# Performance work log

Measured on AMD Instinct MI355X. Metric: run time of the kernel, lower is better.

The kernel has to match this reference:

```python
import jax, jax.numpy as jnp
import numpy as np

B, S, L, D = 16, 1024, 512, 1024
H = 8
DH = D // H
WD = 256          # word/type embedding dim
VOCAB = 1000      # type vocab
NEG = -1e30


def setup_inputs() -> dict:
    key = jax.random.key(0)
    ks = jax.random.split(key, 16)
    inv = 1.0 / np.sqrt(D)
    return {
        "encoder_outs": jax.random.normal(ks[0], (B, S, D), dtype=jnp.float32),
        "to_sem": jax.random.randint(ks[1], (B, L), 0, S, dtype=jnp.int64),
        "to_sem_type": jax.random.randint(ks[2], (B, L), 0, VOCAB, dtype=jnp.int64),
        "sem_syn": jax.random.randint(ks[3], (B, S), 0, L + 1, dtype=jnp.int64),
        "wq": jax.random.normal(ks[4], (D, D), dtype=jnp.float32) * inv,
        "bq": jnp.zeros((D,), dtype=jnp.float32),
        "wk": jax.random.normal(ks[5], (D, D), dtype=jnp.float32) * inv,
        "bk": jnp.zeros((D,), dtype=jnp.float32),
        "wv": jax.random.normal(ks[6], (D, D), dtype=jnp.float32) * inv,
        "bv": jnp.zeros((D,), dtype=jnp.float32),
        "wo": jax.random.normal(ks[7], (D, D), dtype=jnp.float32) * inv,
        "bo": jnp.zeros((D,), dtype=jnp.float32),
        "type_emb": jax.random.normal(ks[8], (VOCAB, WD), dtype=jnp.float32),
        "w_proj": jax.random.normal(ks[9], (D, D + WD), dtype=jnp.float32) / np.sqrt(D + WD),
        "b_proj": jnp.zeros((D,), dtype=jnp.float32),
        "bias_root": jax.random.normal(ks[10], (1, 1, D), dtype=jnp.float32),
    }


def _forward(encoder_outs, to_sem, to_sem_type, sem_syn,
             wq, bq, wk, bk, wv, bv, wo, bo,
             type_emb, w_proj, b_proj, bias_root):
    bsz, len_sem = to_sem.shape
    src_len = encoder_outs.shape[1]

    # batch_index_select: gather the encoder states at semantic head positions
    sem_vec = jnp.take_along_axis(encoder_outs, to_sem[:, :, None], axis=1)  # [B,L,D]

    # Vectorized mask build (replaces the Python loop + scatter):
    # buf[b,i,j] = (sem_syn[b,j] == i+1) or (j == to_sem[b,i])
    ids = jnp.arange(1, len_sem + 1, dtype=sem_syn.dtype)
    aligned = sem_syn[:, None, :] == ids[None, :, None]                       # [B,L,S]
    self_pos = jnp.arange(src_len)[None, None, :] == to_sem[:, :, None]       # [B,L,S]
    allow = aligned | self_pos                                                # [B,L,S]

    # fairseq-style MHA: q scaled by head_dim**-0.5, in/out proj with bias
    q = (sem_vec @ wq.T + bq) * (DH ** -0.5)
    k = encoder_outs @ wk.T + bk
    v = encoder_outs @ wv.T + bv
    q = q.reshape(bsz, len_sem, H, DH)
    k = k.reshape(bsz, src_len, H, DH)
    v = v.reshape(bsz, src_len, H, DH)

    scores = jnp.einsum("blhd,bshd->bhls", q, k)                              # [B,H,L,S]
    scores = jnp.where(allow[:, None, :, :], scores, NEG)
    attn = jax.nn.softmax(scores, axis=-1)
    ctx = jnp.einsum("bhls,bshd->blhd", attn, v).reshape(bsz, len_sem, D)
    sem_vec = ctx @ wo.T + bo                                                 # [B,L,D]

    # arg/type embedding + concat + projection
    type_vec = type_emb[to_sem_type]                                          # [B,L,WD]
    embedding = jnp.concatenate([sem_vec, type_vec], axis=-1) @ w_proj.T + b_proj

    root = jnp.broadcast_to(bias_root, (bsz, 1, D))
    return embedding, jnp.concatenate([root, embedding], axis=1)


def reference(encoder_outs, to_sem, to_sem_type, sem_syn,
              wq, bq, wk, bk, wv, bv, wo, bo,
              type_emb, w_proj, b_proj, bias_root):
    return _forward(encoder_outs, to_sem, to_sem_type, sem_syn,
                    wq, bq, wk, bk, wv, bv, wo, bo,
                    type_emb, w_proj, b_proj, bias_root)
```

## Files before the change

kernel.cpp:

```cpp
#include <hip/hip_runtime.h>

typedef unsigned short u16;
typedef unsigned int   u32;
typedef unsigned long long u64;
typedef __bf16 bf16x8 __attribute__((ext_vector_type(8)));
typedef float  f32x4  __attribute__((ext_vector_type(4)));

#define B_  16
#define S_  1024
#define L_  512
#define D_  1024
#define H_  8
#define WD_ 256
#define KP_ (D_ + WD_)

__device__ __forceinline__ u16 f2bf(float f) {
    u32 u = __float_as_uint(f);
    return (u16)((u + 0x7FFFu + ((u >> 16) & 1u)) >> 16);
}
__device__ __forceinline__ float bf2f(u16 h) {
    return __uint_as_float(((u32)h) << 16);
}
__device__ __forceinline__ void gload16(const void* g, void* l) {
    __builtin_amdgcn_global_load_lds(
        (const __attribute__((address_space(1))) u32*)(unsigned long long)(g),
        (__attribute__((address_space(3))) u32*)(unsigned long long)(l),
        16, 0, 0);
}

__global__ __launch_bounds__(256) void conv_s(const float* __restrict__ x,
                                              u16* __restrict__ y, int n, float s) {
    const int i = (blockIdx.x * 256 + threadIdx.x) * 4;
    if (i < n) {
        const float4 v = *(const float4*)(x + i);
        ushort4 o;
        o.x = f2bf(v.x * s); o.y = f2bf(v.y * s); o.z = f2bf(v.z * s); o.w = f2bf(v.w * s);
        *(ushort4*)(y + i) = o;
    }
}

__global__ __launch_bounds__(256) void conv3_k(
    const float* __restrict__ wk, const float* __restrict__ wv,
    const float* __restrict__ wq, const float* __restrict__ te,
    const float* __restrict__ bk, const float* __restrict__ bv,
    const float* __restrict__ bq,
    u16* __restrict__ wkvq, u16* __restrict__ te_bf,
    float* __restrict__ bkvq, float qs)
{
    const int bid = blockIdx.x;
    if (bid < 3072) {
        const int plane = bid >> 10;
        const int i = ((bid & 1023) * 256 + threadIdx.x) * 4;
        const float* src = plane == 0 ? wk : (plane == 1 ? wv : wq);
        const float s = plane == 2 ? qs : 1.0f;
        const float4 v = *(const float4*)(src + i);
        ushort4 o;
        o.x = f2bf(v.x * s); o.y = f2bf(v.y * s); o.z = f2bf(v.z * s); o.w = f2bf(v.w * s);
        *(ushort4*)(wkvq + (size_t)plane * 1048576 + i) = o;
    } else if (bid < 3322) {
        const int i = ((bid - 3072) * 256 + threadIdx.x) * 4;
        if (i < 256000) {
            const float4 v = *(const float4*)(te + i);
            ushort4 o;
            o.x = f2bf(v.x); o.y = f2bf(v.y); o.z = f2bf(v.z); o.w = f2bf(v.w);
            *(ushort4*)(te_bf + i) = o;
        }
    } else {
        const int i = (bid - 3322) * 1024 + threadIdx.x * 4;
        #pragma unroll
        for (int j = 0; j < 4; ++j) {
            const int idx = i + j;
            bkvq[idx] = (idx < 1024) ? bk[idx]
                      : (idx < 2048 ? bv[idx - 1024] : bq[idx - 2048] * qs);
        }
    }
}

__global__ __launch_bounds__(256) void convT_k(const float* __restrict__ x, u16* __restrict__ y) {
    __shared__ float tile[64][65];
    const int t0 = (blockIdx.x & 15) * 64;
    const int k0 = (blockIdx.x >> 4) * 64;
    const int tr = threadIdx.x >> 4;
    const int tc = threadIdx.x & 15;
    #pragma unroll
    for (int i = 0; i < 4; ++i) {
        const int r = tr + i * 16;
        const float4 v = *(const float4*)(x + (size_t)(t0 + r) * 1024 + k0 + tc * 4);
        tile[r][tc * 4 + 0] = v.x; tile[r][tc * 4 + 1] = v.y;
        tile[r][tc * 4 + 2] = v.z; tile[r][tc * 4 + 3] = v.w;
    }
    __syncthreads();
    #pragma unroll
    for (int i = 0; i < 4; ++i) {
        const int r = tr + i * 16;
        ushort4 o;
        o.x = f2bf(tile[tc * 4 + 0][r]);
        o.y = f2bf(tile[tc * 4 + 1][r]);
        o.z = f2bf(tile[tc * 4 + 2][r]);
        o.w = f2bf(tile[tc * 4 + 3][r]);
        *(ushort4*)(y + (size_t)(k0 + r) * 1024 + t0 + tc * 4) = o;
    }
}

__global__ __launch_bounds__(256) void convP_k(const float* __restrict__ x,
                                               u16* __restrict__ wp1, u16* __restrict__ wfin) {
    const int i = (blockIdx.x * 256 + threadIdx.x) * 4;
    if (i >= 1024 * 1280) return;
    const int n = i / 1280, c = i % 1280;
    const float4 v = *(const float4*)(x + i);
    ushort4 o;
    o.x = f2bf(v.x); o.y = f2bf(v.y); o.z = f2bf(v.z); o.w = f2bf(v.w);
    if (c < 1024) *(ushort4*)(wp1 + (size_t)n * 1024 + c) = o;
    else          *(ushort4*)(wfin + (size_t)n * 1280 + c) = o;
}

__global__ __launch_bounds__(256) void beff_k(const float* __restrict__ wproj,
                                              const float* __restrict__ bo,
                                              const float* __restrict__ bproj,
                                              float* __restrict__ beff) {
    const int w = threadIdx.x >> 6, lane = threadIdx.x & 63;
    const int n = blockIdx.x * 4 + w;
    const float* row = wproj + (size_t)n * 1280;
    float s = 0.f;
    for (int t = lane; t < 1024; t += 64) s += row[t] * bo[t];
    #pragma unroll
    for (int off = 32; off > 0; off >>= 1) s += __shfl_down(s, off);
    if (lane == 0) beff[n] = bproj[n] + s;
}

template <int NT>
__global__ __launch_bounds__(1024, 4) void mm8_k(
    const u16* __restrict__ A, const u16* __restrict__ W,
    const float* __restrict__ bias,
    u16* __restrict__ o0, u16* __restrict__ o1, u16* __restrict__ o2,
    int K, int ntn)
{
    __shared__ alignas(16) u16 lds[65536];
    const int tid  = threadIdx.x;
    const int w    = tid >> 6;
    const int lane = tid & 63;
    const int l15  = lane & 15;
    const int lk   = lane >> 4;
    const int wr   = w >> 2;
    const int wc   = w & 3;

    const int nwg = gridDim.x;
    const int bid = blockIdx.x;
    const int e   = (bid & 7) * (nwg >> 3) + (bid >> 3);
    const int bm0 = (e / ntn) * 256;
    const int bn0 = (e % ntn) * 256;

    const int kc_l = (lane & 3) ^ ((lane >> 3) & 3);
    const u16* gsrc = (w < 8) ? A : W;
    const int rbase = (w < 8) ? bm0 : bn0;
    size_t src[2];
    #pragma unroll
    for (int i = 0; i < 2; ++i) {
        const int row = (w & 7) * 32 + i * 16 + (lane >> 2);
        src[i] = (size_t)(rbase + row) * K + kc_l * 8;
    }
    const int dstA = ((w < 8) ? 0 : 8192) + (w & 7) * 1024;

#define STAGE(t) { u16* d = lds + ((t) & 3) * 16384 + dstA;            \
    gload16(gsrc + src[0] + (size_t)(t) * 32, d);                      \
    gload16(gsrc + src[1] + (size_t)(t) * 32, d + 512); }

    const int rslot = (lk ^ ((l15 >> 1) & 3)) * 8;
    const int aoff = (wr * 64 + l15) * 32 + rslot;
    const int boff = 8192 + (wc * 64 + l15) * 32 + rslot;

    f32x4 acc[4][4] = {};

    STAGE(0); STAGE(1); STAGE(2);
    asm volatile("s_waitcnt vmcnt(4)" ::: "memory");
    __builtin_amdgcn_sched_barrier(0);
    __builtin_amdgcn_s_barrier();

    for (int t = 0; t < NT; ++t) {
        const u16* sa = lds + (t & 3) * 16384 + aoff;
        const u16* sb = lds + (t & 3) * 16384 + boff;
        bf16x8 af[4], bfr[4];
        #pragma unroll
        for (int nf = 0; nf < 4; ++nf) bfr[nf] = *(const bf16x8*)(sb + nf * 512);
        #pragma unroll
        for (int mf = 0; mf < 4; ++mf) af[mf] = *(const bf16x8*)(sa + mf * 512);
        if (t + 3 < NT) STAGE(t + 3);
        __builtin_amdgcn_s_setprio(1);
        #pragma unroll
        for (int mf = 0; mf < 4; ++mf)
            #pragma unroll
            for (int nf = 0; nf < 4; ++nf)
                acc[mf][nf] = __builtin_amdgcn_mfma_f32_16x16x32_bf16(af[mf], bfr[nf], acc[mf][nf], 0, 0, 0);
        __builtin_amdgcn_s_setprio(0);
        if (t < NT - 3)      { asm volatile("s_waitcnt vmcnt(4)" ::: "memory"); }
        else if (t == NT - 3){ asm volatile("s_waitcnt vmcnt(2)" ::: "memory"); }
        else if (t == NT - 2){ asm volatile("s_waitcnt vmcnt(0)" ::: "memory"); }
        __builtin_amdgcn_sched_barrier(0);
        __builtin_amdgcn_s_barrier();
    }
#undef STAGE

    const int plane = bn0 >> 10;
    u16* outp = plane == 0 ? o0 : (plane == 1 ? o1 : o2);
    const int cip0 = (bn0 & 1023) + wc * 64;
    const int colg = bn0 + wc * 64 + l15;
    float bsv[4];
    #pragma unroll
    for (int nf = 0; nf < 4; ++nf) bsv[nf] = bias[colg + nf * 16];
    const int erow = lane >> 3;
    const int echk = lane & 7;
    u16* wlds = lds + w * 2304;

    #pragma unroll
    for (int mf = 0; mf < 4; ++mf) {
        u16* pat = wlds + (mf & 1) * 1152;
        #pragma unroll
        for (int nf = 0; nf < 4; ++nf) {
            #pragma unroll
            for (int r = 0; r < 4; ++r) {
                const float val = acc[mf][nf][r] + bsv[nf];
                const float pv = __shfl_xor(val, 1, 64);
                if ((l15 & 1) == 0) {
                    const u32 pk = (u32)f2bf(val) | ((u32)f2bf(pv) << 16);
                    *(u32*)(pat + (lk * 4 + r) * 72 + nf * 16 + l15) = pk;
                }
            }
        }
        asm volatile("s_waitcnt lgkmcnt(0)" ::: "memory");
        __builtin_amdgcn_sched_barrier(0);
        #pragma unroll
        for (int j2 = 0; j2 < 2; ++j2) {
            const int rr = j2 * 8 + erow;
            const uint4 vv = *(const uint4*)(pat + rr * 72 + echk * 8);
            const int grow = bm0 + wr * 64 + mf * 16 + rr;
            *(uint4*)(outp + (size_t)grow * 1024 + cip0 + echk * 8) = vv;
        }
    }
}

#define AM_PLAIN  0
#define AM_CONCAT 2
#define OM_BF16   0
#define OM_FINAL  1

template <int AMODE, int OMODE>
__global__ __launch_bounds__(256) void mm_k(
    const u16* __restrict__ A, const u16* __restrict__ W,
    const float* __restrict__ bias,
    u16* __restrict__ Ybf, float* __restrict__ Yf, float* __restrict__ Y2,
    int M, int K, int ostride,
    const int* __restrict__ gidx, const u16* __restrict__ aux)
{
    constexpr int N = 1024;
    __shared__ alignas(16) u16 As[4096];
    __shared__ alignas(16) u16 Bs[4096];

    const int tid  = threadIdx.x;
    const int wid  = tid >> 6;
    const int lane = tid & 63;
    const int l15  = lane & 15;
    const int lk   = lane >> 4;

    const int nwg = gridDim.x;
    const int bid = blockIdx.x;
    const int e   = (bid & 7) * (nwg >> 3) + (bid >> 3);
    const int bm0 = (e >> 3) * 128;
    const int bn0 = (e & 7) * 128;

    const int kc_l = (lane & 3) ^ ((lane >> 3) & 3);
    long ga[2], gw[2], gt[2];
    #pragma unroll
    for (int i = 0; i < 2; ++i) {
        const int row = wid * 32 + i * 16 + (lane >> 2);
        if (AMODE == AM_CONCAT) {
            ga[i] = (long)(bm0 + row) * D_ + kc_l * 8;
            gt[i] = (long)gidx[bm0 + row] * WD_ + kc_l * 8;
        } else {
            ga[i] = (long)(bm0 + row) * K + kc_l * 8;
            gt[i] = 0;
        }
        gw[i] = (long)(bn0 + row) * K + kc_l * 8;
    }
    u16* aD = As + wid * 1024;
    u16* bD = Bs + wid * 1024;

    f32x4 acc[4][4] = {};

    const int moff = (wid >> 1) * 64;
    const int noff = (wid & 1) * 64;
    const int rslot = (lk ^ ((l15 >> 1) & 3)) * 8;
    const int aoff = (moff + l15) * 32 + rslot;
    const int boff = (noff + l15) * 32 + rslot;

    for (int k0 = 0; k0 < K; k0 += 32) {
        if (AMODE == AM_CONCAT && k0 >= D_) {
            gload16(aux + gt[0] + (k0 - D_), aD);
            gload16(aux + gt[1] + (k0 - D_), aD + 512);
        } else {
            gload16(A + ga[0] + k0, aD);
            gload16(A + ga[1] + k0, aD + 512);
        }
        gload16(W + gw[0] + k0, bD);
        gload16(W + gw[1] + k0, bD + 512);
        __syncthreads();

        bf16x8 af[4], bfr[4];
        #pragma unroll
        for (int i = 0; i < 4; ++i)
            af[i] = *(const bf16x8*)(As + aoff + i * 512);
        #pragma unroll
        for (int j = 0; j < 4; ++j)
            bfr[j] = *(const bf16x8*)(Bs + boff + j * 512);
        #pragma unroll
        for (int i = 0; i < 4; ++i)
            #pragma unroll
            for (int j = 0; j < 4; ++j)
                acc[i][j] = __builtin_amdgcn_mfma_f32_16x16x32_bf16(af[i], bfr[j], acc[i][j], 0, 0, 0);
        __syncthreads();
    }

    #pragma unroll
    for (int j = 0; j < 4; ++j) {
        const int col = bn0 + noff + j * 16 + l15;
        const float bj = bias ? bias[col] : 0.f;
        #pragma unroll
        for (int i = 0; i < 4; ++i) {
            const int mrow = bm0 + moff + i * 16 + lk * 4;
            #pragma unroll
            for (int r = 0; r < 4; ++r) {
                const float val = acc[i][j][r] + bj;
                const long m = mrow + r;
                if (OMODE == OM_BF16) {
                    Ybf[m * (long)ostride + col] = f2bf(val);
                } else {
                    Yf[m * (long)N + col] = val;
                    const long bb = m >> 9, ll = m & 511;
                    Y2[((bb * (L_ + 1)) + ll + 1) * (long)D_ + col] = val;
                }
            }
        }
    }
}

__global__ __launch_bounds__(256) void attn_k(
    const u16* __restrict__ kb, const u16* __restrict__ vb,
    const int* __restrict__ sem_syn, const int* __restrict__ to_sem,
    const u16* __restrict__ qf, u16* __restrict__ ctx)
{
    __shared__ int   list[S_];
    __shared__ float sc[H_][S_];
    __shared__ int   wcnt[16];

    const int bl  = blockIdx.x;
    const int b   = bl >> 9;
    const int l   = bl & 511;
    const int tid = threadIdx.x;
    const int wvi = tid >> 6;
    const int ln  = tid & 63;

    const int tosem = to_sem[bl];
    const ushort4 qu = *(const ushort4*)(qf + ((size_t)b * S_ + tosem) * D_ + tid * 4);
    const float4 qv = make_float4(bf2f(qu.x), bf2f(qu.y), bf2f(qu.z), bf2f(qu.w));

    bool al[4];
    #pragma unroll
    for (int j = 0; j < 4; ++j) {
        const int s = tid * 4 + j;
        const int a = sem_syn[b * S_ + s];
        al[j] = (a == l + 1) || (s == tosem);
    }
    u64 msk[4];
    #pragma unroll
    for (int j = 0; j < 4; ++j) msk[j] = __ballot(al[j]);
    if (ln == 0) {
        #pragma unroll
        for (int j = 0; j < 4; ++j) wcnt[wvi * 4 + j] = __popcll(msk[j]);
    }
    __syncthreads();
    int mybase[4];
    {
        int tot = 0;
        #pragma unroll
        for (int i2 = 0; i2 < 16; ++i2) {
            const int c2 = wcnt[i2];
            #pragma unroll
            for (int j2 = 0; j2 < 4; ++j2)
                if (i2 == wvi * 4 + j2) mybase[j2] = tot;
            tot += c2;
        }
    }
    const u64 lmlt = (1ull << ln) - 1ull;
    #pragma unroll
    for (int j = 0; j < 4; ++j)
        if (al[j]) list[mybase[j] + __popcll(msk[j] & lmlt)] = tid * 4 + j;
    int n = 0;
    #pragma unroll
    for (int i2 = 0; i2 < 16; ++i2) n += wcnt[i2];
    __syncthreads();

    const int g = tid >> 5;
    const int lane = tid & 31;
    for (int i = 0; i < n; ++i) {
        const u16* krow = kb + ((size_t)b * S_ + list[i]) * D_;
        const ushort4 ku = *(const ushort4*)(krow + tid * 4);
        float p = bf2f(ku.x) * qv.x + bf2f(ku.y) * qv.y + bf2f(ku.z) * qv.z + bf2f(ku.w) * qv.w;
        #pragma unroll
        for (int off = 16; off > 0; off >>= 1) p += __shfl_down(p, off, 32);
        if (lane == 0) sc[g][i] = p;
    }
    __syncthreads();

    float mx = -3.0e38f;
    for (int i = lane; i < n; i += 32) mx = fmaxf(mx, sc[g][i]);
    #pragma unroll
    for (int off = 16; off > 0; off >>= 1) mx = fmaxf(mx, __shfl_xor(mx, off, 32));
    float sum = 0.f;
    for (int i = lane; i < n; i += 32) {
        const float e = expf(sc[g][i] - mx);
        sc[g][i] = e;
        sum += e;
    }
    #pragma unroll
    for (int off = 16; off > 0; off >>= 1) sum += __shfl_xor(sum, off, 32);
    const float inv = 1.0f / sum;
    __syncthreads();

    float4 a4 = make_float4(0.f, 0.f, 0.f, 0.f);
    for (int i = 0; i < n; ++i) {
        const float wgt = sc[g][i] * inv;
        const u16* vrow = vb + ((size_t)b * S_ + list[i]) * D_;
        const ushort4 vu = *(const ushort4*)(vrow + tid * 4);
        a4.x = fmaf(wgt, bf2f(vu.x), a4.x);
        a4.y = fmaf(wgt, bf2f(vu.y), a4.y);
        a4.z = fmaf(wgt, bf2f(vu.z), a4.z);
        a4.w = fmaf(wgt, bf2f(vu.w), a4.w);
    }
    ushort4 o;
    o.x = f2bf(a4.x); o.y = f2bf(a4.y); o.z = f2bf(a4.z); o.w = f2bf(a4.w);
    *(ushort4*)(ctx + (size_t)bl * D_ + tid * 4) = o;
}

__global__ __launch_bounds__(256) void root_k(
    const float* __restrict__ broot, float* __restrict__ out2)
{
    const int i = blockIdx.x * 256 + threadIdx.x;
    const int b = i >> 10, d = i & 1023;
    out2[(size_t)b * (L_ + 1) * D_ + d] = broot[d];
}

extern "C" void kernel_launch(void* const* d_in, const int* in_sizes, int n_in,
                              void* d_out, int out_size, void* d_ws, size_t ws_size,
                              hipStream_t stream)
{
    const float* enc    = (const float*)d_in[0];
    const int*   to_sem = (const int*)  d_in[1];
    const int*   tstype = (const int*)  d_in[2];
    const int*   semsyn = (const int*)  d_in[3];
    const float* wq = (const float*)d_in[4];
    const float* bq = (const float*)d_in[5];
    const float* wk = (const float*)d_in[6];
    const float* bk = (const float*)d_in[7];
    const float* wv = (const float*)d_in[8];
    const float* bv = (const float*)d_in[9];
    const float* wo = (const float*)d_in[10];
    const float* bo = (const float*)d_in[11];
    const float* temb  = (const float*)d_in[12];
    const float* wproj = (const float*)d_in[13];
    const float* bproj = (const float*)d_in[14];
    const float* broot = (const float*)d_in[15];

    float* out1 = (float*)d_out;
    float* out2 = out1 + (size_t)B_ * L_ * D_;

    unsigned char* ws = (unsigned char*)d_ws;
    u16*   enc_bf = (u16*)(ws);
    u16*   k_bf   = (u16*)(ws + (32ull << 20));
    u16*   wkvq   = (u16*)(ws + (64ull << 20));
    u16*   wot    = (u16*)(ws + (70ull << 20));
    u16*   wp1    = (u16*)(ws + (72ull << 20));
    u16*   wfin   = (u16*)(ws + (74ull << 20));
    float* beff   = (float*)(ws + (77ull << 20));
    float* bkvq   = (float*)(ws + (77ull << 20) + 8192);
    u16*   ctx_bf = (u16*)(ws + (78ull << 20));
    u16*   te_bf  = (u16*)(ws + (94ull << 20));

    u16* v_bf = (u16*)d_out;
    u16* q_bf = (u16*)((unsigned char*)d_out + (32ull << 20));

    const float qscale = 0.08838834764831845f;
    dim3 blk(256);

    conv_s<<<dim3(16384), blk, 0, stream>>>(enc, enc_bf, 16777216, 1.0f);
    conv3_k<<<dim3(3325), blk, 0, stream>>>(wk, wv, wq, temb, bk, bv, bq,
                                            wkvq, te_bf, bkvq, qscale);
    convT_k<<<dim3(256),  blk, 0, stream>>>(wo, wot);
    convP_k<<<dim3(1280), blk, 0, stream>>>(wproj, wp1, wfin);
    beff_k<<<dim3(256),   blk, 0, stream>>>(wproj, bo, bproj, beff);

    mm8_k<32><<<dim3(768), dim3(1024), 0, stream>>>(
        enc_bf, wkvq, bkvq, k_bf, v_bf, q_bf, 1024, 12);

    mm_k<AM_PLAIN, OM_BF16><<<dim3(64), blk, 0, stream>>>(
        wp1, wot, nullptr, wfin, nullptr, nullptr, 1024, 1024, 1280, nullptr, nullptr);

    attn_k<<<dim3(B_ * L_), blk, 0, stream>>>(k_bf, v_bf, semsyn, to_sem, q_bf, ctx_bf);

    mm_k<AM_CONCAT, OM_FINAL><<<dim3(512), blk, 0, stream>>>(
        ctx_bf, wfin, beff, nullptr, out1, out2, B_ * L_, KP_, 1024, tstype, te_bf);

    root_k<<<dim3((B_ * D_) / 256), blk, 0, stream>>>(broot, out2);
}
```

Baseline: 240.0 us.

## Switch QKV GEMM to 32x32x16 MFMA with split-K register double buffering

```diff
diff --git a/kernel.cpp b/kernel.cpp
--- a/kernel.cpp
+++ b/kernel.cpp
@@ -5,6 +5,7 @@
 typedef unsigned long long u64;
 typedef __bf16 bf16x8 __attribute__((ext_vector_type(8)));
 typedef float  f32x4  __attribute__((ext_vector_type(4)));
+typedef float  f32x16 __attribute__((ext_vector_type(16)));
 
 #define B_  16
 #define S_  1024
@@ -139,8 +140,8 @@
     const int tid  = threadIdx.x;
     const int w    = tid >> 6;
     const int lane = tid & 63;
-    const int l15  = lane & 15;
-    const int lk   = lane >> 4;
+    const int l31  = lane & 31;
+    const int khalf= lane >> 5;
     const int wr   = w >> 2;
     const int wc   = w & 3;
 
@@ -165,75 +166,91 @@
     gload16(gsrc + src[0] + (size_t)(t) * 32, d);                      \
     gload16(gsrc + src[1] + (size_t)(t) * 32, d + 512); }
 
-    const int rslot = (lk ^ ((l15 >> 1) & 3)) * 8;
-    const int aoff = (wr * 64 + l15) * 32 + rslot;
-    const int boff = 8192 + (wc * 64 + l15) * 32 + rslot;
-
-    f32x4 acc[4][4] = {};
+    const int rA = wr * 64 + l31;
+    const int rB = wc * 64 + l31;
+    const int sA0 = khalf ^ ((rA >> 1) & 3);
+    const int sB0 = khalf ^ ((rB >> 1) & 3);
+    const int aH0 = rA * 32 + sA0 * 8;
+    const int aH1 = rA * 32 + (sA0 ^ 2) * 8;
+    const int bH0 = 8192 + rB * 32 + sB0 * 8;
+    const int bH1 = 8192 + rB * 32 + (sB0 ^ 2) * 8;
+
+    f32x16 acc00 = {}, acc01 = {}, acc10 = {}, acc11 = {};
+    bf16x8 a0_0, a0_1, b0_0, b0_1;
+    bf16x8 a1_0, a1_1, b1_0, b1_1;
 
     STAGE(0); STAGE(1); STAGE(2);
     asm volatile("s_waitcnt vmcnt(4)" ::: "memory");
     __builtin_amdgcn_sched_barrier(0);
     __builtin_amdgcn_s_barrier();
+    __builtin_amdgcn_sched_barrier(0);
+    a0_0 = *(const bf16x8*)(lds + aH0);
+    a0_1 = *(const bf16x8*)(lds + aH0 + 1024);
+    b0_0 = *(const bf16x8*)(lds + bH0);
+    b0_1 = *(const bf16x8*)(lds + bH0 + 1024);
 
     for (int t = 0; t < NT; ++t) {
-        const u16* sa = lds + (t & 3) * 16384 + aoff;
-        const u16* sb = lds + (t & 3) * 16384 + boff;
-        bf16x8 af[4], bfr[4];
-        #pragma unroll
-        for (int nf = 0; nf < 4; ++nf) bfr[nf] = *(const bf16x8*)(sb + nf * 512);
-        #pragma unroll
-        for (int mf = 0; mf < 4; ++mf) af[mf] = *(const bf16x8*)(sa + mf * 512);
+        const int sb = (t & 3) * 16384;
+        a1_0 = *(const bf16x8*)(lds + sb + aH1);
+        a1_1 = *(const bf16x8*)(lds + sb + aH1 + 1024);
+        b1_0 = *(const bf16x8*)(lds + sb + bH1);
+        b1_1 = *(const bf16x8*)(lds + sb + bH1 + 1024);
         if (t + 3 < NT) STAGE(t + 3);
         __builtin_amdgcn_s_setprio(1);
-        #pragma unroll
-        for (int mf = 0; mf < 4; ++mf)
-            #pragma unroll
-            for (int nf = 0; nf < 4; ++nf)
-                acc[mf][nf] = __builtin_amdgcn_mfma_f32_16x16x32_bf16(af[mf], bfr[nf], acc[mf][nf], 0, 0, 0);
+        acc00 = __builtin_amdgcn_mfma_f32_32x32x16_bf16(a0_0, b0_0, acc00, 0, 0, 0);
+        acc01 = __builtin_amdgcn_mfma_f32_32x32x16_bf16(a0_0, b0_1, acc01, 0, 0, 0);
+        acc10 = __builtin_amdgcn_mfma_f32_32x32x16_bf16(a0_1, b0_0, acc10, 0, 0, 0);
+        acc11 = __builtin_amdgcn_mfma_f32_32x32x16_bf16(a0_1, b0_1, acc11, 0, 0, 0);
         __builtin_amdgcn_s_setprio(0);
         if (t < NT - 3)      { asm volatile("s_waitcnt vmcnt(4)" ::: "memory"); }
         else if (t == NT - 3){ asm volatile("s_waitcnt vmcnt(2)" ::: "memory"); }
         else if (t == NT - 2){ asm volatile("s_waitcnt vmcnt(0)" ::: "memory"); }
         __builtin_amdgcn_sched_barrier(0);
         __builtin_amdgcn_s_barrier();
+        __builtin_amdgcn_sched_barrier(0);
+        if (t + 1 < NT) {
+            const int sb2 = ((t + 1) & 3) * 16384;
+            a0_0 = *(const bf16x8*)(lds + sb2 + aH0);
+            a0_1 = *(const bf16x8*)(lds + sb2 + aH0 + 1024);
+            b0_0 = *(const bf16x8*)(lds + sb2 + bH0);
+            b0_1 = *(const bf16x8*)(lds + sb2 + bH0 + 1024);
+        }
+        __builtin_amdgcn_s_setprio(1);
+        acc00 = __builtin_amdgcn_mfma_f32_32x32x16_bf16(a1_0, b1_0, acc00, 0, 0, 0);
+        acc01 = __builtin_amdgcn_mfma_f32_32x32x16_bf16(a1_0, b1_1, acc01, 0, 0, 0);
+        acc10 = __builtin_amdgcn_mfma_f32_32x32x16_bf16(a1_1, b1_0, acc10, 0, 0, 0);
+        acc11 = __builtin_amdgcn_mfma_f32_32x32x16_bf16(a1_1, b1_1, acc11, 0, 0, 0);
+        __builtin_amdgcn_s_setprio(0);
+        __builtin_amdgcn_s_barrier();
+        __builtin_amdgcn_sched_barrier(0);
     }
 #undef STAGE
 
     const int plane = bn0 >> 10;
     u16* outp = plane == 0 ? o0 : (plane == 1 ? o1 : o2);
     const int cip0 = (bn0 & 1023) + wc * 64;
-    const int colg = bn0 + wc * 64 + l15;
-    float bsv[4];
-    #pragma unroll
-    for (int nf = 0; nf < 4; ++nf) bsv[nf] = bias[colg + nf * 16];
-    const int erow = lane >> 3;
-    const int echk = lane & 7;
-    u16* wlds = lds + w * 2304;
-
-    #pragma unroll
-    for (int mf = 0; mf < 4; ++mf) {
-        u16* pat = wlds + (mf & 1) * 1152;
-        #pragma unroll
-        for (int nf = 0; nf < 4; ++nf) {
+    const float bsv0 = bias[bn0 + wc * 64 + l31];
+    const float bsv1 = bias[bn0 + wc * 64 + 32 + l31];
+    const int rowbase = bm0 + wr * 64 + 4 * khalf;
+
+    #pragma unroll
+    for (int fm = 0; fm < 2; ++fm) {
+        #pragma unroll
+        for (int fn = 0; fn < 2; ++fn) {
+            const f32x16 frag = fm == 0 ? (fn == 0 ? acc00 : acc01)
+                                        : (fn == 0 ? acc10 : acc11);
+            const float bs = fn == 0 ? bsv0 : bsv1;
+            const int gcol = cip0 + fn * 32 + l31;
             #pragma unroll
-            for (int r = 0; r < 4; ++r) {
-                const float val = acc[mf][nf][r] + bsv[nf];
+            for (int r = 0; r < 16; ++r) {
+                const float val = frag[r] + bs;
                 const float pv = __shfl_xor(val, 1, 64);
-                if ((l15 & 1) == 0) {
+                if ((lane & 1) == 0) {
                     const u32 pk = (u32)f2bf(val) | ((u32)f2bf(pv) << 16);
-                    *(u32*)(pat + (lk * 4 + r) * 72 + nf * 16 + l15) = pk;
+                    const int grow = rowbase + fm * 32 + (r & 3) + 8 * (r >> 2);
+                    *(u32*)(outp + (size_t)grow * 1024 + gcol) = pk;
                 }
             }
-        }
-        asm volatile("s_waitcnt lgkmcnt(0)" ::: "memory");
-        __builtin_amdgcn_sched_barrier(0);
-        #pragma unroll
-        for (int j2 = 0; j2 < 2; ++j2) {
-            const int rr = j2 * 8 + erow;
-            const uint4 vv = *(const uint4*)(pat + rr * 72 + echk * 8);
-            const int grow = bm0 + wr * 64 + mf * 16 + rr;
-            *(uint4*)(outp + (size_t)grow * 1024 + cip0 + echk * 8) = vv;
         }
     }
 }
```

After: 254.6 us. 1.06x slower.

## Software-pipeline mm_k with a 4-stage LDS ring and merge conversion kernels

Applied to the files above, without the earlier changes.

```diff
diff --git a/kernel.cpp b/kernel.cpp
--- a/kernel.cpp
+++ b/kernel.cpp
@@ -28,37 +28,34 @@
         16, 0, 0);
 }
 
-__global__ __launch_bounds__(256) void conv_s(const float* __restrict__ x,
-                                              u16* __restrict__ y, int n, float s) {
-    const int i = (blockIdx.x * 256 + threadIdx.x) * 4;
-    if (i < n) {
-        const float4 v = *(const float4*)(x + i);
-        ushort4 o;
-        o.x = f2bf(v.x * s); o.y = f2bf(v.y * s); o.z = f2bf(v.z * s); o.w = f2bf(v.w * s);
-        *(ushort4*)(y + i) = o;
-    }
-}
-
-__global__ __launch_bounds__(256) void conv3_k(
+__global__ __launch_bounds__(256) void convA_k(
+    const float* __restrict__ enc,
     const float* __restrict__ wk, const float* __restrict__ wv,
     const float* __restrict__ wq, const float* __restrict__ te,
     const float* __restrict__ bk, const float* __restrict__ bv,
     const float* __restrict__ bq,
-    u16* __restrict__ wkvq, u16* __restrict__ te_bf,
+    u16* __restrict__ enc_bf, u16* __restrict__ wkvq, u16* __restrict__ te_bf,
     float* __restrict__ bkvq, float qs)
 {
     const int bid = blockIdx.x;
-    if (bid < 3072) {
-        const int plane = bid >> 10;
-        const int i = ((bid & 1023) * 256 + threadIdx.x) * 4;
+    if (bid < 16384) {
+        const int i = (bid * 256 + threadIdx.x) * 4;
+        const float4 v = *(const float4*)(enc + i);
+        ushort4 o;
+        o.x = f2bf(v.x); o.y = f2bf(v.y); o.z = f2bf(v.z); o.w = f2bf(v.w);
+        *(ushort4*)(enc_bf + i) = o;
+    } else if (bid < 19456) {
+        const int b2 = bid - 16384;
+        const int plane = b2 >> 10;
+        const int i = ((b2 & 1023) * 256 + threadIdx.x) * 4;
         const float* src = plane == 0 ? wk : (plane == 1 ? wv : wq);
         const float s = plane == 2 ? qs : 1.0f;
         const float4 v = *(const float4*)(src + i);
         ushort4 o;
         o.x = f2bf(v.x * s); o.y = f2bf(v.y * s); o.z = f2bf(v.z * s); o.w = f2bf(v.w * s);
         *(ushort4*)(wkvq + (size_t)plane * 1048576 + i) = o;
-    } else if (bid < 3322) {
-        const int i = ((bid - 3072) * 256 + threadIdx.x) * 4;
+    } else if (bid < 19706) {
+        const int i = ((bid - 19456) * 256 + threadIdx.x) * 4;
         if (i < 256000) {
             const float4 v = *(const float4*)(te + i);
             ushort4 o;
@@ -66,7 +63,7 @@
             *(ushort4*)(te_bf + i) = o;
         }
     } else {
-        const int i = (bid - 3322) * 1024 + threadIdx.x * 4;
+        const int i = (bid - 19706) * 1024 + threadIdx.x * 4;
         #pragma unroll
         for (int j = 0; j < 4; ++j) {
             const int idx = i + j;
@@ -243,17 +240,16 @@
 #define OM_BF16   0
 #define OM_FINAL  1
 
-template <int AMODE, int OMODE>
+template <int NT, int AMODE, int OMODE>
 __global__ __launch_bounds__(256) void mm_k(
     const u16* __restrict__ A, const u16* __restrict__ W,
     const float* __restrict__ bias,
     u16* __restrict__ Ybf, float* __restrict__ Yf, float* __restrict__ Y2,
-    int M, int K, int ostride,
+    int K, int ostride,
     const int* __restrict__ gidx, const u16* __restrict__ aux)
 {
     constexpr int N = 1024;
-    __shared__ alignas(16) u16 As[4096];
-    __shared__ alignas(16) u16 Bs[4096];
+    __shared__ alignas(16) u16 lds[32768];
 
     const int tid  = threadIdx.x;
     const int wid  = tid >> 6;
@@ -281,8 +277,19 @@
         }
         gw[i] = (long)(bn0 + row) * K + kc_l * 8;
     }
-    u16* aD = As + wid * 1024;
-    u16* bD = Bs + wid * 1024;
+
+#define MSTAGE(t) { const int k0t = (t) * 32;                              \
+    u16* d  = lds + ((t) & 3) * 8192 + wid * 1024;                         \
+    u16* db = d + 4096;                                                    \
+    if (AMODE == AM_CONCAT && k0t >= D_) {                                 \
+        gload16(aux + gt[0] + (k0t - D_), d);                              \
+        gload16(aux + gt[1] + (k0t - D_), d + 512);                        \
+    } else {                                                               \
+        gload16(A + ga[0] + k0t, d);                                       \
+        gload16(A + ga[1] + k0t, d + 512);                                 \
+    }                                                                      \
+    gload16(W + gw[0] + k0t, db);                                          \
+    gload16(W + gw[1] + k0t, db + 512); }
 
     f32x4 acc[4][4] = {};
 
@@ -290,34 +297,36 @@
     const int noff = (wid & 1) * 64;
     const int rslot = (lk ^ ((l15 >> 1) & 3)) * 8;
     const int aoff = (moff + l15) * 32 + rslot;
-    const int boff = (noff + l15) * 32 + rslot;
-
-    for (int k0 = 0; k0 < K; k0 += 32) {
-        if (AMODE == AM_CONCAT && k0 >= D_) {
-            gload16(aux + gt[0] + (k0 - D_), aD);
-            gload16(aux + gt[1] + (k0 - D_), aD + 512);
-        } else {
-            gload16(A + ga[0] + k0, aD);
-            gload16(A + ga[1] + k0, aD + 512);
-        }
-        gload16(W + gw[0] + k0, bD);
-        gload16(W + gw[1] + k0, bD + 512);
-        __syncthreads();
-
+    const int boff = 4096 + (noff + l15) * 32 + rslot;
+
+    MSTAGE(0); MSTAGE(1); MSTAGE(2);
+    asm volatile("s_waitcnt vmcnt(8)" ::: "memory");
+    __builtin_amdgcn_sched_barrier(0);
+    __builtin_amdgcn_s_barrier();
+
+    for (int t = 0; t < NT; ++t) {
+        const u16* sa = lds + (t & 3) * 8192 + aoff;
+        const u16* sb = lds + (t & 3) * 8192 + boff;
         bf16x8 af[4], bfr[4];
         #pragma unroll
-        for (int i = 0; i < 4; ++i)
-            af[i] = *(const bf16x8*)(As + aoff + i * 512);
-        #pragma unroll
-        for (int j = 0; j < 4; ++j)
-            bfr[j] = *(const bf16x8*)(Bs + boff + j * 512);
+        for (int j = 0; j < 4; ++j) bfr[j] = *(const bf16x8*)(sb + j * 512);
+        #pragma unroll
+        for (int i = 0; i < 4; ++i) af[i] = *(const bf16x8*)(sa + i * 512);
+        if (t + 3 < NT) MSTAGE(t + 3);
+        __builtin_amdgcn_s_setprio(1);
         #pragma unroll
         for (int i = 0; i < 4; ++i)
             #pragma unroll
             for (int j = 0; j < 4; ++j)
                 acc[i][j] = __builtin_amdgcn_mfma_f32_16x16x32_bf16(af[i], bfr[j], acc[i][j], 0, 0, 0);
-        __syncthreads();
-    }
+        __builtin_amdgcn_s_setprio(0);
+        if (t < NT - 3)      { asm volatile("s_waitcnt vmcnt(8)" ::: "memory"); }
+        else if (t == NT - 3){ asm volatile("s_waitcnt vmcnt(4)" ::: "memory"); }
+        else if (t == NT - 2){ asm volatile("s_waitcnt vmcnt(0)" ::: "memory"); }
+        __builtin_amdgcn_sched_barrier(0);
+        __builtin_amdgcn_s_barrier();
+    }
+#undef MSTAGE
 
     #pragma unroll
     for (int j = 0; j < 4; ++j) {
@@ -490,9 +499,8 @@
     const float qscale = 0.08838834764831845f;
     dim3 blk(256);
 
-    conv_s<<<dim3(16384), blk, 0, stream>>>(enc, enc_bf, 16777216, 1.0f);
-    conv3_k<<<dim3(3325), blk, 0, stream>>>(wk, wv, wq, temb, bk, bv, bq,
-                                            wkvq, te_bf, bkvq, qscale);
+    convA_k<<<dim3(19709), blk, 0, stream>>>(enc, wk, wv, wq, temb, bk, bv, bq,
+                                             enc_bf, wkvq, te_bf, bkvq, qscale);
     convT_k<<<dim3(256),  blk, 0, stream>>>(wo, wot);
     convP_k<<<dim3(1280), blk, 0, stream>>>(wproj, wp1, wfin);
     beff_k<<<dim3(256),   blk, 0, stream>>>(wproj, bo, bproj, beff);
@@ -500,13 +508,13 @@
     mm8_k<32><<<dim3(768), dim3(1024), 0, stream>>>(
         enc_bf, wkvq, bkvq, k_bf, v_bf, q_bf, 1024, 12);
 
-    mm_k<AM_PLAIN, OM_BF16><<<dim3(64), blk, 0, stream>>>(
-        wp1, wot, nullptr, wfin, nullptr, nullptr, 1024, 1024, 1280, nullptr, nullptr);
+    mm_k<32, AM_PLAIN, OM_BF16><<<dim3(64), blk, 0, stream>>>(
+        wp1, wot, nullptr, wfin, nullptr, nullptr, 1024, 1280, nullptr, nullptr);
 
     attn_k<<<dim3(B_ * L_), blk, 0, stream>>>(k_bf, v_bf, semsyn, to_sem, q_bf, ctx_bf);
 
-    mm_k<AM_CONCAT, OM_FINAL><<<dim3(512), blk, 0, stream>>>(
-        ctx_bf, wfin, beff, nullptr, out1, out2, B_ * L_, KP_, 1024, tstype, te_bf);
+    mm_k<40, AM_CONCAT, OM_FINAL><<<dim3(512), blk, 0, stream>>>(
+        ctx_bf, wfin, beff, nullptr, out1, out2, KP_, 1024, tstype, te_bf);
 
     root_k<<<dim3((B_ * D_) / 256), blk, 0, stream>>>(broot, out2);
 }
```

New measurement: 227.1 us. -5.4%, faster.
